# Performance work log

Hardware: AMD Instinct MI355X
Metric: run time of the kernel (lower is better)

## Reference

```python
import jax, jax.numpy as jnp
import numpy as np

Z, Y, X = 200, 8, 200
XM, YM, ZM = 80.0, 6.0, 80.0  # x_meter, y_meter, z_meter
IMG_H, IMG_W = 256, 512
FEAT_C, OUT_CH = 64, 128
EPS = 1e-8


def create_grid3d():
    # matches torch create_grid3d flattening order (z, y, x), x/y shifted by -0.5
    zz, yy, xx = jnp.meshgrid(jnp.linspace(0.0, 1.0, Z),
                              jnp.linspace(0.0, 1.0, Y),
                              jnp.linspace(0.0, 1.0, X), indexing='ij')
    xyz = jnp.stack([xx.ravel() - 0.5, yy.ravel() - 0.5, zz.ravel()], axis=1)  # (N,3)
    return xyz * jnp.array([XM, YM, ZM], dtype=jnp.float32)


def setup_inputs() -> dict:
    key = jax.random.key(0)
    k1, k2, k3 = jax.random.split(key, 3)
    B = 2
    img_feat = jax.random.normal(k1, (B, FEAT_C, 32, 64), dtype=jnp.float32)
    # realistic pinhole intrinsics so many voxels project in-bounds
    K = jnp.array([[300.0, 0.0, IMG_W / 2.0],
                   [0.0, 300.0, IMG_H / 2.0],
                   [0.0, 0.0, 1.0]], dtype=jnp.float32)
    pix_T_cam = jnp.tile(K[None], (B, 1, 1))
    conv_w = jax.random.normal(k2, (OUT_CH, FEAT_C * Y), dtype=jnp.float32) * 0.02
    conv_b = jax.random.normal(k3, (OUT_CH,), dtype=jnp.float32) * 0.02
    return {"img_feat": img_feat, "pix_T_cam": pix_T_cam, "conv_w": conv_w, "conv_b": conv_b}


def reference(img_feat, pix_T_cam, conv_w, conv_b):
    B, C, H, W = img_feat.shape
    xyz = create_grid3d()  # (N,3), N = Z*Y*X
    pix = jnp.einsum('bij,nj->bni', pix_T_cam, xyz)  # (B,N,3)
    d = pix[..., 2]
    u01 = pix[..., 0] / (d + EPS) / IMG_W  # normalized [0,1] u
    v01 = pix[..., 1] / (d + EPS) / IMG_H
    valid = (u01 >= 0) & (v01 >= 0) & (u01 <= 1) & (v01 <= 1)  # (B,N)

    # grid_sample, align_corners=False, padding_mode='zeros' (D=1 collapses to bilinear)
    gx = u01 * 2.0 - 1.0
    gy = v01 * 2.0 - 1.0
    xp = ((gx + 1.0) * W - 1.0) * 0.5
    yp = ((gy + 1.0) * H - 1.0) * 0.5
    x0f = jnp.floor(xp); y0f = jnp.floor(yp)
    wx1 = xp - x0f; wy1 = yp - y0f
    x0 = x0f.astype(jnp.int32); y0 = y0f.astype(jnp.int32)
    bidx = jnp.arange(B)[:, None]

    def gather(xi, yi):
        ok = (xi >= 0) & (xi < W) & (yi >= 0) & (yi < H)
        xc = jnp.clip(xi, 0, W - 1)
        yc = jnp.clip(yi, 0, H - 1)
        vals = img_feat[bidx, :, yc, xc]  # (B,N,C)
        return vals * ok[..., None].astype(img_feat.dtype)

    v00 = gather(x0, y0)
    v01_ = gather(x0 + 1, y0)
    v10 = gather(x0, y0 + 1)
    v11 = gather(x0 + 1, y0 + 1)
    samp = (v00 * ((1 - wx1) * (1 - wy1))[..., None]
            + v01_ * (wx1 * (1 - wy1))[..., None]
            + v10 * ((1 - wx1) * wy1)[..., None]
            + v11 * (wx1 * wy1)[..., None])  # (B,N,C)
    samp = samp * valid[..., None].astype(samp.dtype)

    bev = samp.reshape(B, Z, Y, X, C)
    # rearrange 'b c d h w -> b (c h) d w' with d=Z, h=Y, w=X
    bev = jnp.transpose(bev, (0, 4, 2, 1, 3)).reshape(B, C * Y, Z, X)
    out = jnp.einsum('bczx,oc->bozx', bev, conv_w) + conv_b[None, :, None, None]
    return out
```

## Files before the change

kernel.cpp:

```cpp
#include <hip/hip_runtime.h>


#define NPOS 40000

typedef short bf16x8 __attribute__((ext_vector_type(8)));
typedef float f32x4  __attribute__((ext_vector_type(4)));

__device__ __forceinline__ unsigned rne16(float f) {
    unsigned u = __float_as_uint(f);
    return (u + 0x7fffu + ((u >> 16) & 1u)) >> 16;
}
__device__ __forceinline__ float lo16(unsigned u) { return __uint_as_float(u << 16); }
__device__ __forceinline__ float hi16(unsigned u) { return __uint_as_float(u & 0xffff0000u); }
__device__ __forceinline__ unsigned cvtpk(float lo, float hi) {
    unsigned r;
    asm("v_cvt_pk_bf16_f32 %0, %1, %2" : "=v"(r) : "v"(lo), "v"(hi));
    return r;
}

__global__ __launch_bounds__(256)
void bili_prep(const float* __restrict__ img, const float* __restrict__ convw,
               unsigned short* __restrict__ imgT, unsigned short* __restrict__ Wp)
{
    const int i = blockIdx.x * 256 + threadIdx.x;
    if (blockIdx.x < 1024) {
        const int c = i & 63, x = (i >> 6) & 63, y = (i >> 12) & 31, b = i >> 17;
        imgT[i] = (unsigned short)rne16(img[((b * 64 + c) * 32 + y) * 64 + x]);
    } else {
        const int j = i - 1024 * 256;
        const int k = j & 511, o = j >> 9;
        const int y = k >> 6, c = k & 63;
        Wp[j] = (unsigned short)rne16(convw[o * 512 + c * 8 + y]);
    }
}

__global__ __launch_bounds__(256, 2)
void bili_main(const uint4* __restrict__ imgTq,
               const unsigned short* __restrict__ Wp,
               const float* __restrict__ pixT,
               const float* __restrict__ convb,
               float* __restrict__ out)
{
    __shared__ uint4  Fb[2][1024];
    __shared__ uint2  offsC[512];
    __shared__ float4 wtsL[512];

    const int t   = threadIdx.x;
    const int bx  = blockIdx.x;
    const int b   = (bx >= 625) ? 1 : 0;
    const int n0  = (bx - b * 625) * 64;

    const int wv  = t >> 6;
    const int ln  = t & 63;
    const int l15 = ln & 15;
    const int lg  = ln >> 4;
    const int g   = t >> 3;
    const int li  = t & 7;

    float bias0[4], bias1[4];
    #pragma unroll
    for (int r = 0; r < 4; ++r) {
        bias0[r] = convb[wv * 32 +      lg * 4 + r];
        bias1[r] = convb[wv * 32 + 16 + lg * 4 + r];
    }
    f32x4 acc0[4], acc1[4];
    #pragma unroll
    for (int nt = 0; nt < 4; ++nt)
        #pragma unroll
        for (int r = 0; r < 4; ++r) { acc0[nt][r] = bias0[r]; acc1[nt][r] = bias1[r]; }

    {
        const float* Kb = pixT + b * 9;
        const float K00 = Kb[0], K01 = Kb[1], K02 = Kb[2];
        const float K10 = Kb[3], K11 = Kb[4], K12 = Kb[5];
        const float K20 = Kb[6], K21 = Kb[7], K22 = Kb[8];

        #pragma unroll
        for (int r = 0; r < 2; ++r) {
            const int p    = r * 256 + t;
            const int nloc = p >> 3;
            const int y    = p & 7;
            const int n = n0 + nloc;
            const int z = n / 200;
            const int x = n - z * 200;

            const float pxv = (x * (1.0f / 199.0f) - 0.5f) * 80.0f;
            const float pzv = (z * (1.0f / 199.0f)) * 80.0f;
            const float pyv = (y * (1.0f / 7.0f) - 0.5f) * 6.0f;

            const float p0 = K00 * pxv + K01 * pyv + K02 * pzv;
            const float p1 = K10 * pxv + K11 * pyv + K12 * pzv;
            const float d  = K20 * pxv + K21 * pyv + K22 * pzv;
            const float dpe = d + 1e-8f;
            const float u01 = p0 / dpe / 512.0f;
            const float v01 = p1 / dpe / 256.0f;
            const float vf = (u01 >= 0.0f && u01 <= 1.0f &&
                              v01 >= 0.0f && v01 <= 1.0f) ? 1.0f : 0.0f;

            float xp = u01 * 64.0f - 0.5f;
            xp = fminf(fmaxf(xp, -2.0f), 66.0f);
            const float x0f = floorf(xp);
            const float wx = xp - x0f;
            const int x0 = (int)x0f, x1i = x0 + 1;
            const float wx0 = (1.0f - wx) * vf * ((x0  >= 0 && x0  < 64) ? 1.0f : 0.0f);
            const float wx1 = wx          * vf * ((x1i >= 0 && x1i < 64) ? 1.0f : 0.0f);
            const int xi0 = min(max(x0, 0), 63);
            const int xi1 = min(max(x1i, 0), 63);

            float yp = v01 * 32.0f - 0.5f;
            yp = fminf(fmaxf(yp, -2.0f), 34.0f);
            const float y0f = floorf(yp);
            const float wy = yp - y0f;
            const int y0 = (int)y0f, y1i = y0 + 1;
            const float wy0 = (1.0f - wy) * ((y0  >= 0 && y0  < 32) ? 1.0f : 0.0f);
            const float wy1 = wy          * ((y1i >= 0 && y1i < 32) ? 1.0f : 0.0f);
            const int yi0 = min(max(y0, 0), 31);
            const int yi1 = min(max(y1i, 0), 31);

            const unsigned o0 = (unsigned)(((yi0 << 6) + xi0) << 3);
            const unsigned o1 = (unsigned)(((yi0 << 6) + xi1) << 3);
            const unsigned o2 = (unsigned)(((yi1 << 6) + xi0) << 3);
            const unsigned o3 = (unsigned)(((yi1 << 6) + xi1) << 3);

            wtsL[p]  = make_float4(wx0 * wy0, wx1 * wy0, wx0 * wy1, wx1 * wy1);
            offsC[p] = make_uint2(o0 | (o1 << 16), o2 | (o3 << 16));
        }
    }

    __syncthreads();

    const uint4*  imgTb = imgTq + b * 16384;
    const bf16x8* ApG   = (const bf16x8*)Wp;
    const bf16x8* Ap0   = ApG + ((wv * 32 +      l15) * 64 + lg);
    const bf16x8* Ap1   = ApG + ((wv * 32 + 16 + l15) * 64 + lg);

    uint4  sbuf[16];
    float4 wreg[4];

    #define ISSUE(q)                                                           \
        _Pragma("unroll")                                                      \
        for (int it = 0; it < 4; ++it) {                                       \
            const int pp = it * 32 + g;                                        \
            const int n_ = pp >> 1, ys = pp & 1;                               \
            const int p_ = n_ * 8 + 2 * (q) + ys;                              \
            const uint2 oc = offsC[p_];                                        \
            wreg[it] = wtsL[p_];                                               \
            sbuf[it * 4 + 0] = imgTb[(oc.x & 0xffffu) + li];                   \
            sbuf[it * 4 + 1] = imgTb[(oc.x >> 16)     + li];                   \
            sbuf[it * 4 + 2] = imgTb[(oc.y & 0xffffu) + li];                   \
            sbuf[it * 4 + 3] = imgTb[(oc.y >> 16)     + li];                   \
        }

    #define MFMAQ(q, buf)                                                      \
        do {                                                                   \
            bf16x8 a0_[4], a1_[4];                                             \
            _Pragma("unroll")                                                  \
            for (int k = 0; k < 4; ++k) {                                      \
                a0_[k] = Ap0[((q) * 4 + k) * 4];                               \
                a1_[k] = Ap1[((q) * 4 + k) * 4];                               \
            }                                                                  \
            const bf16x8* Fv = (const bf16x8*)(buf);                           \
            _Pragma("unroll")                                                  \
            for (int k = 0; k < 4; ++k) {                                      \
                _Pragma("unroll")                                              \
                for (int nt = 0; nt < 4; ++nt) {                               \
                    const int nn = nt * 16 + l15;                              \
                    const bf16x8 bv = Fv[nn * 16 + ((k * 4 + lg) ^ (nn & 7))]; \
                    acc0[nt] = __builtin_amdgcn_mfma_f32_16x16x32_bf16(a0_[k], bv, acc0[nt], 0, 0, 0); \
                    acc1[nt] = __builtin_amdgcn_mfma_f32_16x16x32_bf16(a1_[k], bv, acc1[nt], 0, 0, 0); \
                }                                                              \
            }                                                                  \
        } while (0)

    #define PROCESS(q, buf)                                                    \
        _Pragma("unroll")                                                      \
        for (int it = 0; it < 4; ++it) {                                       \
            const int pp = it * 32 + g;                                        \
            const int n_ = pp >> 1, ys = pp & 1;                               \
            const float4 w = wreg[it];                                         \
            float2 ac[4];                                                      \
            _Pragma("unroll")                                                  \
            for (int qq = 0; qq < 4; ++qq) ac[qq] = make_float2(0.0f, 0.0f);   \
            _Pragma("unroll")                                                  \
            for (int j = 0; j < 4; ++j) {                                      \
                const uint4 v = sbuf[it * 4 + j];                              \
                const float ww = (j == 0) ? w.x : (j == 1) ? w.y : (j == 2) ? w.z : w.w; \
                ac[0].x = fmaf(ww, lo16(v.x), ac[0].x);                        \
                ac[0].y = fmaf(ww, hi16(v.x), ac[0].y);                        \
                ac[1].x = fmaf(ww, lo16(v.y), ac[1].x);                        \
                ac[1].y = fmaf(ww, hi16(v.y), ac[1].y);                        \
                ac[2].x = fmaf(ww, lo16(v.z), ac[2].x);                        \
                ac[2].y = fmaf(ww, hi16(v.z), ac[2].y);                        \
                ac[3].x = fmaf(ww, lo16(v.w), ac[3].x);                        \
                ac[3].y = fmaf(ww, hi16(v.w), ac[3].y);                        \
            }                                                                  \
            uint4 pk;                                                          \
            pk.x = cvtpk(ac[0].x, ac[0].y);                                    \
            pk.y = cvtpk(ac[1].x, ac[1].y);                                    \
            pk.z = cvtpk(ac[2].x, ac[2].y);                                    \
            pk.w = cvtpk(ac[3].x, ac[3].y);                                    \
            (buf)[n_ * 16 + ((ys * 8 + li) ^ (n_ & 7))] = pk;                  \
        }

    ISSUE(0);                 PROCESS(0, Fb[0]); __syncthreads();
    ISSUE(1); MFMAQ(0, Fb[0]); PROCESS(1, Fb[1]); __syncthreads();
    ISSUE(2); MFMAQ(1, Fb[1]); PROCESS(2, Fb[0]); __syncthreads();
    ISSUE(3); MFMAQ(2, Fb[0]); PROCESS(3, Fb[1]); __syncthreads();
    MFMAQ(3, Fb[1]);

    #undef ISSUE
    #undef MFMAQ
    #undef PROCESS

    {
        float* ob = out + (size_t)(b * 128 + wv * 32) * NPOS + n0;
        #pragma unroll
        for (int nt = 0; nt < 4; ++nt) {
            #pragma unroll
            for (int r = 0; r < 4; ++r) {
                ob[(     lg * 4 + r) * NPOS + nt * 16 + l15] = acc0[nt][r];
                ob[(16 + lg * 4 + r) * NPOS + nt * 16 + l15] = acc1[nt][r];
            }
        }
    }
}

extern "C" void kernel_launch(void* const* d_in, const int* in_sizes, int n_in,
                              void* d_out, int out_size, void* d_ws, size_t ws_size,
                              hipStream_t stream) {
    const float* img   = (const float*)d_in[0];
    const float* pixT  = (const float*)d_in[1];
    const float* convw = (const float*)d_in[2];
    const float* convb = (const float*)d_in[3];
    float* out = (float*)d_out;

    unsigned short* imgT = (unsigned short*)d_ws;
    unsigned short* Wp   = imgT + 262144;

    hipLaunchKernelGGL(bili_prep, dim3(1280), dim3(256), 0, stream,
                       img, convw, imgT, Wp);
    hipLaunchKernelGGL(bili_main, dim3(1250), dim3(256), 0, stream,
                       (const uint4*)imgT, Wp, pixT, convb, out);
}
```

Before: 44.19 us.

## Split gather/MFMA stages into half-steps and raise occupancy to three blocks

Breaks each quarter's gather, blend and MFMA stages into two halves that use separate even and odd register buffers, so the gather loads of the next half are issued while the current half is blended and multiplied. This lowers live register pressure, which lets launch bounds ask for three blocks per SM instead of two. It also swaps the two divisions in the projection for one hardware reciprocal, and reloads the bilinear weights from LDS instead of holding them in registers. The trade-off is slightly different rounding from the approximate reciprocal, possible spills under the tighter register cap, and a finer interleave whose benefit depends on how the compiler schedules it.

```diff
diff --git a/kernel.cpp b/kernel.cpp
--- a/kernel.cpp
+++ b/kernel.cpp
@@ -34,7 +34,7 @@
     }
 }
 
-__global__ __launch_bounds__(256, 2)
+__global__ __launch_bounds__(256, 3)
 void bili_main(const uint4* __restrict__ imgTq,
                const unsigned short* __restrict__ Wp,
                const float* __restrict__ pixT,
@@ -57,17 +57,19 @@
     const int g   = t >> 3;
     const int li  = t & 7;
 
-    float bias0[4], bias1[4];
-    #pragma unroll
-    for (int r = 0; r < 4; ++r) {
-        bias0[r] = convb[wv * 32 +      lg * 4 + r];
-        bias1[r] = convb[wv * 32 + 16 + lg * 4 + r];
-    }
     f32x4 acc0[4], acc1[4];
-    #pragma unroll
-    for (int nt = 0; nt < 4; ++nt)
-        #pragma unroll
-        for (int r = 0; r < 4; ++r) { acc0[nt][r] = bias0[r]; acc1[nt][r] = bias1[r]; }
+    {
+        float bias0[4], bias1[4];
+        #pragma unroll
+        for (int r = 0; r < 4; ++r) {
+            bias0[r] = convb[wv * 32 +      lg * 4 + r];
+            bias1[r] = convb[wv * 32 + 16 + lg * 4 + r];
+        }
+        #pragma unroll
+        for (int nt = 0; nt < 4; ++nt)
+            #pragma unroll
+            for (int r = 0; r < 4; ++r) { acc0[nt][r] = bias0[r]; acc1[nt][r] = bias1[r]; }
+    }
 
     {
         const float* Kb = pixT + b * 9;
@@ -91,9 +93,9 @@
             const float p0 = K00 * pxv + K01 * pyv + K02 * pzv;
             const float p1 = K10 * pxv + K11 * pyv + K12 * pzv;
             const float d  = K20 * pxv + K21 * pyv + K22 * pzv;
-            const float dpe = d + 1e-8f;
-            const float u01 = p0 / dpe / 512.0f;
-            const float v01 = p1 / dpe / 256.0f;
+            const float inv = __builtin_amdgcn_rcpf(d + 1e-8f);
+            const float u01 = p0 * inv * (1.0f / 512.0f);
+            const float v01 = p1 * inv * (1.0f / 256.0f);
             const float vf = (u01 >= 0.0f && u01 <= 1.0f &&
                               v01 >= 0.0f && v01 <= 1.0f) ? 1.0f : 0.0f;
 
@@ -134,56 +136,34 @@
     const bf16x8* Ap0   = ApG + ((wv * 32 +      l15) * 64 + lg);
     const bf16x8* Ap1   = ApG + ((wv * 32 + 16 + l15) * 64 + lg);
 
-    uint4  sbuf[16];
-    float4 wreg[4];
-
-    #define ISSUE(q)                                                           \
+    uint4 sbE[8], sbO[8];
+
+    #define ISSUE_H(q, hb, SB)                                                 \
         _Pragma("unroll")                                                      \
-        for (int it = 0; it < 4; ++it) {                                       \
-            const int pp = it * 32 + g;                                        \
+        for (int it2 = 0; it2 < 2; ++it2) {                                    \
+            const int pp = ((hb) * 2 + it2) * 32 + g;                          \
             const int n_ = pp >> 1, ys = pp & 1;                               \
             const int p_ = n_ * 8 + 2 * (q) + ys;                              \
             const uint2 oc = offsC[p_];                                        \
-            wreg[it] = wtsL[p_];                                               \
-            sbuf[it * 4 + 0] = imgTb[(oc.x & 0xffffu) + li];                   \
-            sbuf[it * 4 + 1] = imgTb[(oc.x >> 16)     + li];                   \
-            sbuf[it * 4 + 2] = imgTb[(oc.y & 0xffffu) + li];                   \
-            sbuf[it * 4 + 3] = imgTb[(oc.y >> 16)     + li];                   \
-        }
-
-    #define MFMAQ(q, buf)                                                      \
-        do {                                                                   \
-            bf16x8 a0_[4], a1_[4];                                             \
-            _Pragma("unroll")                                                  \
-            for (int k = 0; k < 4; ++k) {                                      \
-                a0_[k] = Ap0[((q) * 4 + k) * 4];                               \
-                a1_[k] = Ap1[((q) * 4 + k) * 4];                               \
-            }                                                                  \
-            const bf16x8* Fv = (const bf16x8*)(buf);                           \
-            _Pragma("unroll")                                                  \
-            for (int k = 0; k < 4; ++k) {                                      \
-                _Pragma("unroll")                                              \
-                for (int nt = 0; nt < 4; ++nt) {                               \
-                    const int nn = nt * 16 + l15;                              \
-                    const bf16x8 bv = Fv[nn * 16 + ((k * 4 + lg) ^ (nn & 7))]; \
-                    acc0[nt] = __builtin_amdgcn_mfma_f32_16x16x32_bf16(a0_[k], bv, acc0[nt], 0, 0, 0); \
-                    acc1[nt] = __builtin_amdgcn_mfma_f32_16x16x32_bf16(a1_[k], bv, acc1[nt], 0, 0, 0); \
-                }                                                              \
-            }                                                                  \
-        } while (0)
-
-    #define PROCESS(q, buf)                                                    \
+            SB[it2 * 4 + 0] = imgTb[(oc.x & 0xffffu) + li];                    \
+            SB[it2 * 4 + 1] = imgTb[(oc.x >> 16)     + li];                    \
+            SB[it2 * 4 + 2] = imgTb[(oc.y & 0xffffu) + li];                    \
+            SB[it2 * 4 + 3] = imgTb[(oc.y >> 16)     + li];                    \
+        }
+
+    #define PROC_H(q, hb, SB, buf)                                             \
         _Pragma("unroll")                                                      \
-        for (int it = 0; it < 4; ++it) {                                       \
-            const int pp = it * 32 + g;                                        \
+        for (int it2 = 0; it2 < 2; ++it2) {                                    \
+            const int pp = ((hb) * 2 + it2) * 32 + g;                          \
             const int n_ = pp >> 1, ys = pp & 1;                               \
-            const float4 w = wreg[it];                                         \
+            const int p_ = n_ * 8 + 2 * (q) + ys;                              \
+            const float4 w = wtsL[p_];                                         \
             float2 ac[4];                                                      \
             _Pragma("unroll")                                                  \
             for (int qq = 0; qq < 4; ++qq) ac[qq] = make_float2(0.0f, 0.0f);   \
             _Pragma("unroll")                                                  \
             for (int j = 0; j < 4; ++j) {                                      \
-                const uint4 v = sbuf[it * 4 + j];                              \
+                const uint4 v = SB[it2 * 4 + j];                               \
                 const float ww = (j == 0) ? w.x : (j == 1) ? w.y : (j == 2) ? w.z : w.w; \
                 ac[0].x = fmaf(ww, lo16(v.x), ac[0].x);                        \
                 ac[0].y = fmaf(ww, hi16(v.x), ac[0].y);                        \
@@ -202,15 +182,60 @@
             (buf)[n_ * 16 + ((ys * 8 + li) ^ (n_ & 7))] = pk;                  \
         }
 
-    ISSUE(0);                 PROCESS(0, Fb[0]); __syncthreads();
-    ISSUE(1); MFMAQ(0, Fb[0]); PROCESS(1, Fb[1]); __syncthreads();
-    ISSUE(2); MFMAQ(1, Fb[1]); PROCESS(2, Fb[0]); __syncthreads();
-    ISSUE(3); MFMAQ(2, Fb[0]); PROCESS(3, Fb[1]); __syncthreads();
-    MFMAQ(3, Fb[1]);
-
-    #undef ISSUE
-    #undef MFMAQ
-    #undef PROCESS
+    #define MFMA_H(q, hf, buf)                                                 \
+        do {                                                                   \
+            const bf16x8* Fv = (const bf16x8*)(buf);                           \
+            _Pragma("unroll")                                                  \
+            for (int k2 = 0; k2 < 2; ++k2) {                                   \
+                const int k = (hf) * 2 + k2;                                   \
+                const bf16x8 a0_ = Ap0[((q) * 4 + k) * 4];                     \
+                const bf16x8 a1_ = Ap1[((q) * 4 + k) * 4];                     \
+                _Pragma("unroll")                                              \
+                for (int nt = 0; nt < 4; ++nt) {                               \
+                    const int nn = nt * 16 + l15;                              \
+                    const bf16x8 bv = Fv[nn * 16 + ((k * 4 + lg) ^ (nn & 7))]; \
+                    acc0[nt] = __builtin_amdgcn_mfma_f32_16x16x32_bf16(a0_, bv, acc0[nt], 0, 0, 0); \
+                    acc1[nt] = __builtin_amdgcn_mfma_f32_16x16x32_bf16(a1_, bv, acc1[nt], 0, 0, 0); \
+                }                                                              \
+            }                                                                  \
+        } while (0)
+
+    ISSUE_H(0, 0, sbE);
+    ISSUE_H(0, 1, sbO);
+    PROC_H (0, 0, sbE, Fb[0]);
+    ISSUE_H(1, 0, sbE);
+    PROC_H (0, 1, sbO, Fb[0]);
+    __syncthreads();
+
+    ISSUE_H(1, 1, sbO);
+    MFMA_H (0, 0, Fb[0]);
+    PROC_H (1, 0, sbE, Fb[1]);
+    ISSUE_H(2, 0, sbE);
+    MFMA_H (0, 1, Fb[0]);
+    PROC_H (1, 1, sbO, Fb[1]);
+    __syncthreads();
+
+    ISSUE_H(2, 1, sbO);
+    MFMA_H (1, 0, Fb[1]);
+    PROC_H (2, 0, sbE, Fb[0]);
+    ISSUE_H(3, 0, sbE);
+    MFMA_H (1, 1, Fb[1]);
+    PROC_H (2, 1, sbO, Fb[0]);
+    __syncthreads();
+
+    ISSUE_H(3, 1, sbO);
+    MFMA_H (2, 0, Fb[0]);
+    PROC_H (3, 0, sbE, Fb[1]);
+    MFMA_H (2, 1, Fb[0]);
+    PROC_H (3, 1, sbO, Fb[1]);
+    __syncthreads();
+
+    MFMA_H (3, 0, Fb[1]);
+    MFMA_H (3, 1, Fb[1]);
+
+    #undef ISSUE_H
+    #undef PROC_H
+    #undef MFMA_H
 
     {
         float* ob = out + (size_t)(b * 128 + wv * 32) * NPOS + n0;
```

After: 43.56 us. About the same (-1.4%).
